# Kernel optimization log

Hardware: AMD Instinct MI355X
Metric: run time of the kernel (lower is better)

## Reference

```python
import jax, jax.numpy as jnp
import numpy as np

S_LOCAL = 3
N_HEADS = 8
EPS = 1e-6


def setup_inputs() -> dict:
    key = jax.random.key(0)
    ks = jax.random.split(key, 9)
    B, D, T, H, W = 2, 512, 96, 16, 16
    std = 0.02
    return {
        "x": jax.random.normal(ks[0], (B, D, T, H, W), dtype=jnp.float32),
        "ln_gamma": jnp.ones((D,), dtype=jnp.float32),
        "ln_beta": jnp.zeros((D,), dtype=jnp.float32),
        "Wq": jax.random.normal(ks[1], (D, D), dtype=jnp.float32) * std,
        "Wk": jax.random.normal(ks[2], (D, D), dtype=jnp.float32) * std,
        "Wv": jax.random.normal(ks[3], (D, D), dtype=jnp.float32) * std,
        "Wkl": jax.random.normal(ks[4], (D, D), dtype=jnp.float32) * std,
        "Wvl": jax.random.normal(ks[5], (D, D), dtype=jnp.float32) * std,
        "Wo": jax.random.normal(ks[6], (D, D), dtype=jnp.float32) * std,
        "q_bias": jax.random.normal(ks[7], (1, N_HEADS, 1, D // N_HEADS), dtype=jnp.float32) * std,
    }


def _unfold_windows(x, s):
    # x: [..., T] -> [..., T, s] sliding windows with zero padding s//2 each side
    p = s // 2
    xp = jnp.pad(x, [(0, 0)] * (x.ndim - 1) + [(p, p)])
    T = x.shape[-1]
    idx = jnp.arange(T)[:, None] + jnp.arange(s)[None, :]  # [T, s]
    return xp[..., idx]


def reference(x, ln_gamma, ln_beta, Wq, Wk, Wv, Wkl, Wvl, Wo, q_bias):
    B, D, T, H, W = x.shape
    nh, dh, s = N_HEADS, D // N_HEADS, S_LOCAL
    factor = dh ** (-0.5)
    N = B * H * W

    # [B,D,T,H,W] -> [N, T, D]
    xt = jnp.transpose(x, (0, 3, 4, 2, 1)).reshape(N, T, D)

    # LayerNorm over D
    mu = xt.mean(-1, keepdims=True)
    var = xt.var(-1, keepdims=True)
    xn = (xt - mu) / jnp.sqrt(var + EPS) * ln_gamma + ln_beta

    # projections -> [N, nh, T, dh]
    def heads(y):
        return jnp.transpose(y.reshape(N, T, nh, dh), (0, 2, 1, 3))

    q = heads(xn @ Wq.T) + q_bias
    k = heads(xn @ Wk.T)
    v = heads(xn @ Wv.T)

    # global attention scores [N, nh, T, T]
    attn_global = jnp.einsum('bhnd,bhgd->bhng', q, k) * factor

    # local k/v: [N, T, D] -> [N, D, T] -> windows [N, D, T, s]
    kl = jnp.transpose(xn @ Wkl.T, (0, 2, 1))
    vl = jnp.transpose(xn @ Wvl.T, (0, 2, 1))
    k_w = jnp.transpose(_unfold_windows(kl, s).reshape(N, nh, dh, T, s), (0, 1, 3, 2, 4))  # [N,nh,T,dh,s]
    v_w = jnp.transpose(_unfold_windows(vl, s).reshape(N, nh, dh, T, s), (0, 1, 3, 2, 4))

    # local mask: True where window element came from zero padding -> [T, s]
    mask_local = _unfold_windows(jnp.ones((T,), dtype=jnp.float32), s) == 0

    attn_local = jnp.einsum('bhnd,bhndl->bhnl', q, k_w)
    attn_local = jnp.where(mask_local, -jnp.inf, attn_local) * factor

    # joint softmax over [T global + s local]
    attn_map = jax.nn.softmax(jnp.concatenate([attn_global, attn_local], axis=-1), axis=-1)
    ag, al = attn_map[..., :T], attn_map[..., T:]

    x_global = jnp.einsum('bhng,bhgd->bhnd', ag, v)
    x_local = jnp.einsum('bhnl,bhndl->bhnd', al, v_w)

    out = (jnp.transpose(x_global + x_local, (0, 2, 1, 3)).reshape(N, T, D)) @ Wo.T
    return jnp.transpose(out.reshape(B, H, W, T, D), (0, 4, 3, 1, 2))
```

## Files before the change

kernel.cpp:

```cpp
#include <hip/hip_runtime.h>
#include <hip/hip_fp16.h>
#include <cstdint>
#include <cstddef>

typedef _Float16 f16;
typedef _Float16 half8 __attribute__((ext_vector_type(8)));
typedef _Float16 half4v __attribute__((ext_vector_type(4)));
typedef float floatx4 __attribute__((ext_vector_type(4)));

#define MTOT 49152
#define QSCALE 0.180336880111120426f

__device__ __forceinline__ void gload_lds16(const f16* g, f16* l) {
  __builtin_amdgcn_global_load_lds((const __attribute__((address_space(1))) void*)g,
                                   (__attribute__((address_space(3))) void*)l, 16, 0, 0);
}

__device__ __forceinline__ half8 load_h8u(const f16* p) {
  half8 v;
  __builtin_memcpy(&v, p, 16);
  return v;
}

__global__ __launch_bounds__(256) void wconv_kernel(
    const float* __restrict__ Wq, const float* __restrict__ Wk,
    const float* __restrict__ Wv, const float* __restrict__ Wkl,
    const float* __restrict__ Wvl, const float* __restrict__ Wo,
    f16* __restrict__ WQKV, f16* __restrict__ WO) {
  int idx = blockIdx.x * 256 + threadIdx.x;
  if (idx < 2560 * 512) {
    int row = idx >> 9;
    int col = idx & 511;
    int seg = row >> 9;
    int r = row & 511;
    const float* src;
    switch (seg) {
      case 0: src = Wq; break;
      case 1: src = Wk; break;
      case 2: src = Wkl; break;
      case 3: src = Wvl; break;
      default: src = Wv; break;
    }
    WQKV[idx] = (f16)src[r * 512 + col];
  }
  if (idx < 512 * 512) WO[idx] = (f16)Wo[idx];
}

__global__ __launch_bounds__(256) void ln_kernel(
    const float* __restrict__ x, const float* __restrict__ gamma,
    const float* __restrict__ beta, f16* __restrict__ XN) {
  const int hwg = blockIdx.x & 3;
  const int t   = (blockIdx.x >> 2) % 96;
  const int b   = blockIdx.x / (4 * 96);
  const int lhw = threadIdx.x & 63;
  const int dg  = threadIdx.x >> 6;
  const int hw  = hwg * 64 + lhw;
  const float* xp = x + (size_t)b * 512 * 24576 + (size_t)t * 256 + hw +
                    (size_t)dg * 128 * 24576;

  float v[128];
  float s = 0.f, s2 = 0.f;
#pragma unroll
  for (int j = 0; j < 128; ++j) {
    float u = xp[(size_t)j * 24576];
    v[j] = u;
    s += u;
    s2 += u * u;
  }
  __shared__ float S1[4][64], S2[4][64];
  S1[dg][lhw] = s;
  S2[dg][lhw] = s2;
  __syncthreads();
  s  = S1[0][lhw] + S1[1][lhw] + S1[2][lhw] + S1[3][lhw];
  s2 = S2[0][lhw] + S2[1][lhw] + S2[2][lhw] + S2[3][lhw];
  const float mean = s * (1.f / 512.f);
  float var = s2 * (1.f / 512.f) - mean * mean;
  var = fmaxf(var, 0.f);
  const float rstd = rsqrtf(var + 1e-6f);
  const int n = b * 256 + hw;
  f16* outp = XN + ((size_t)n * 96 + t) * 512 + dg * 128;
#pragma unroll
  for (int d0 = 0; d0 < 128; d0 += 8) {
    half8 buf;
#pragma unroll
    for (int j = 0; j < 8; ++j) {
      const int d = dg * 128 + d0 + j;
      buf[j] = (f16)((v[d0 + j] - mean) * rstd * gamma[d] + beta[d]);
    }
    *(half8*)(outp + d0) = buf;
  }
}

__global__ __launch_bounds__(512, 2) void gemmA_kernel(
    const f16* __restrict__ A, const f16* __restrict__ B,
    f16* __restrict__ Cqkv, const float* __restrict__ qbias) {
  __shared__ f16 LA[2][256 * 64];
  __shared__ f16 LB[2][256 * 64];
  __shared__ __align__(16) f16 esc[8][16][72];

  const int lin = blockIdx.x;
  const int cpx = (int)gridDim.x >> 3;
  const int swz = (lin & 7) * cpx + (lin >> 3);
  const int o = ((gridDim.x & 7) == 0) ? swz : lin;
  const int mt = o / 10;
  const int nt = o % 10;
  const int m0 = mt * 256;
  const int n0 = nt * 256;

  const int tid = threadIdx.x;
  const int wid = tid >> 6;
  const int lane = tid & 63;
  const int wm = wid >> 2;
  const int wn = wid & 3;
  const int l15 = lane & 15, l4 = lane >> 4;

  const int srow = tid >> 3;
  const int scol = ((tid & 7) ^ (srow & 7)) * 8;
  const f16* Abase = A + (size_t)(m0 + srow) * 512 + scol;
  const f16* Bbase = B + (size_t)(n0 + srow) * 512 + scol;

  const int cks0 = ((l4) ^ (l15 & 7)) * 8;
  const int cks1 = ((4 + l4) ^ (l15 & 7)) * 8;
  const int arow = wm * 128 + l15;
  const int brow = wn * 64 + l15;

  floatx4 acc[8][4] = {};
  half8 a_f[4][2];
  half8 b_f[4][2];

  auto stageH = [&](int slot, int kt, int mat, int h) {
    const f16* g = (mat ? Bbase : Abase) + kt * 64 + (size_t)(h * 128) * 512;
    f16* l = (mat ? LB[slot] : LA[slot]) + h * 8192 + tid * 8;
    gload_lds16(g, l);
    gload_lds16(g + (size_t)64 * 512, l + 4096);
  };

  stageH(0, 0, 0, 0); stageH(0, 0, 0, 1);
  stageH(0, 0, 1, 0); stageH(0, 0, 1, 1);
  stageH(1, 1, 0, 0);
  asm volatile("s_waitcnt vmcnt(2)" ::: "memory");
  __builtin_amdgcn_s_barrier();

#pragma unroll
  for (int kt = 0; kt < 8; ++kt) {
    const f16* As = LA[kt & 1];
    const f16* Bs = LB[kt & 1];
    const int nsl = (kt + 1) & 1;

#pragma unroll
    for (int mf2 = 0; mf2 < 4; ++mf2) {
      a_f[mf2][0] = *(const half8*)(As + (arow + mf2 * 16) * 64 + cks0);
      a_f[mf2][1] = *(const half8*)(As + (arow + mf2 * 16) * 64 + cks1);
    }
#pragma unroll
    for (int nf = 0; nf < 2; ++nf) {
      b_f[nf][0] = *(const half8*)(Bs + (brow + nf * 16) * 64 + cks0);
      b_f[nf][1] = *(const half8*)(Bs + (brow + nf * 16) * 64 + cks1);
    }
    if (kt + 1 < 8) stageH(nsl, kt + 1, 0, 1);
    __builtin_amdgcn_s_barrier();
    __builtin_amdgcn_s_setprio(1);
#pragma unroll
    for (int mf2 = 0; mf2 < 4; ++mf2)
#pragma unroll
      for (int nf2 = 0; nf2 < 2; ++nf2)
#pragma unroll
        for (int ks = 0; ks < 2; ++ks)
          acc[mf2][nf2] = __builtin_amdgcn_mfma_f32_16x16x32_f16(
              a_f[mf2][ks], b_f[nf2][ks], acc[mf2][nf2], 0, 0, 0);
    __builtin_amdgcn_s_setprio(0);
    __builtin_amdgcn_s_barrier();

#pragma unroll
    for (int nf = 2; nf < 4; ++nf) {
      b_f[nf][0] = *(const half8*)(Bs + (brow + nf * 16) * 64 + cks0);
      b_f[nf][1] = *(const half8*)(Bs + (brow + nf * 16) * 64 + cks1);
    }
    if (kt + 1 < 8) stageH(nsl, kt + 1, 1, 0);
    __builtin_amdgcn_s_barrier();
    __builtin_amdgcn_s_setprio(1);
#pragma unroll
    for (int mf2 = 0; mf2 < 4; ++mf2)
#pragma unroll
      for (int nf2 = 0; nf2 < 2; ++nf2)
#pragma unroll
        for (int ks = 0; ks < 2; ++ks)
          acc[mf2][2 + nf2] = __builtin_amdgcn_mfma_f32_16x16x32_f16(
              a_f[mf2][ks], b_f[2 + nf2][ks], acc[mf2][2 + nf2], 0, 0, 0);
    __builtin_amdgcn_s_setprio(0);
    __builtin_amdgcn_s_barrier();

#pragma unroll
    for (int mf2 = 0; mf2 < 4; ++mf2) {
      a_f[mf2][0] = *(const half8*)(As + (arow + 64 + mf2 * 16) * 64 + cks0);
      a_f[mf2][1] = *(const half8*)(As + (arow + 64 + mf2 * 16) * 64 + cks1);
    }
    if (kt + 1 < 8) stageH(nsl, kt + 1, 1, 1);
    __builtin_amdgcn_s_barrier();
    __builtin_amdgcn_s_setprio(1);
#pragma unroll
    for (int mf2 = 0; mf2 < 4; ++mf2)
#pragma unroll
      for (int nf2 = 0; nf2 < 2; ++nf2)
#pragma unroll
        for (int ks = 0; ks < 2; ++ks)
          acc[4 + mf2][nf2] = __builtin_amdgcn_mfma_f32_16x16x32_f16(
              a_f[mf2][ks], b_f[nf2][ks], acc[4 + mf2][nf2], 0, 0, 0);
    __builtin_amdgcn_s_setprio(0);
    __builtin_amdgcn_s_barrier();

    if (kt + 2 < 8) stageH(kt & 1, kt + 2, 0, 0);
    __builtin_amdgcn_s_barrier();
    __builtin_amdgcn_s_setprio(1);
#pragma unroll
    for (int mf2 = 0; mf2 < 4; ++mf2)
#pragma unroll
      for (int nf2 = 0; nf2 < 2; ++nf2)
#pragma unroll
        for (int ks = 0; ks < 2; ++ks)
          acc[4 + mf2][2 + nf2] = __builtin_amdgcn_mfma_f32_16x16x32_f16(
              a_f[mf2][ks], b_f[2 + nf2][ks], acc[4 + mf2][2 + nf2], 0, 0, 0);
    __builtin_amdgcn_s_setprio(0);
    if (kt < 6) {
      asm volatile("s_waitcnt vmcnt(2)" ::: "memory");
    } else if (kt == 6) {
      asm volatile("s_waitcnt vmcnt(0)" ::: "memory");
    }
    __builtin_amdgcn_s_barrier();
  }

  float bias[4], scl[4];
#pragma unroll
  for (int nf = 0; nf < 4; ++nf) {
    const int n = n0 + wn * 64 + nf * 16 + l15;
    const bool isq = (n < 512);
    bias[nf] = isq ? qbias[n] : 0.0f;
    scl[nf]  = isq ? QSCALE : 1.0f;
  }
  const int rrow = lane >> 2;
  const int rcg  = lane & 3;
#pragma unroll
  for (int mf = 0; mf < 8; ++mf) {
#pragma unroll
    for (int nf = 0; nf < 4; ++nf)
#pragma unroll
      for (int j = 0; j < 4; ++j)
        esc[wid][l4 * 4 + j][nf * 16 + l15] = (f16)((acc[mf][nf][j] + bias[nf]) * scl[nf]);
    asm volatile("s_waitcnt lgkmcnt(0)" ::: "memory");
    half8 v0 = *(const half8*)(&esc[wid][rrow][rcg * 16]);
    half8 v1 = *(const half8*)(&esc[wid][rrow][rcg * 16 + 8]);
    asm volatile("" ::: "memory");
    f16* dst = Cqkv + (size_t)(m0 + wm * 128 + mf * 16 + rrow) * 2560 + n0 + wn * 64 + rcg * 16;
    *(half8*)dst = v0;
    *(half8*)(dst + 8) = v1;
  }
}

__global__ __launch_bounds__(256) void gemmO_kernel(
    const f16* __restrict__ A, const f16* __restrict__ B,
    float* __restrict__ Out) {
  __shared__ f16 As[2][128 * 32];
  __shared__ f16 Bs[2][128 * 32];

  const int lin = blockIdx.x;
  const int cpx = (int)gridDim.x >> 3;
  const int o = (lin & 7) * cpx + (lin >> 3);
  const int nt = o >> 2;
  const int mt = o & 3;
  const int m0 = mt * 128;
  const int n0 = nt * 128;
  const int tid = threadIdx.x;
  const int lane = tid & 63;
  const int wid = tid >> 6;
  const int wm = wid >> 1, wn = wid & 1;
  const int l15 = lane & 15, l4 = lane >> 4;

  floatx4 acc[4][4] = {};

  const int srow = tid >> 2;
  const int skp = (((tid & 3) ^ ((tid >> 3) & 3))) * 8;
  const f16* ap = A + (size_t)(m0 + srow) * 512 + skp;
  const f16* bp = B + (size_t)(n0 + srow) * 512 + skp;

  auto stage = [&](int buf, int k0) {
    f16* asl = As[buf] + tid * 8;
    f16* bsl = Bs[buf] + tid * 8;
    gload_lds16(ap + k0, asl);
    gload_lds16(ap + (size_t)64 * 512 + k0, asl + 2048);
    gload_lds16(bp + k0, bsl);
    gload_lds16(bp + (size_t)64 * 512 + k0, bsl + 2048);
  };

  const int rc = (l4 ^ ((l15 >> 1) & 3)) * 8;

  stage(0, 0);
  __syncthreads();
  int cur = 0;
  for (int k0 = 0; k0 < 512; k0 += 32) {
    if (k0 + 32 < 512) stage(cur ^ 1, k0 + 32);
    half8 af[4], bf[4];
#pragma unroll
    for (int mf = 0; mf < 4; ++mf)
      af[mf] = *(const half8*)(As[cur] + (wm * 64 + mf * 16 + l15) * 32 + rc);
#pragma unroll
    for (int nf = 0; nf < 4; ++nf)
      bf[nf] = *(const half8*)(Bs[cur] + (wn * 64 + nf * 16 + l15) * 32 + rc);
#pragma unroll
    for (int mf = 0; mf < 4; ++mf)
#pragma unroll
      for (int nf = 0; nf < 4; ++nf)
        acc[mf][nf] = __builtin_amdgcn_mfma_f32_16x16x32_f16(af[mf], bf[nf], acc[mf][nf], 0, 0, 0);
    __syncthreads();
    cur ^= 1;
  }

  const int mbase = m0 + wm * 64;
  const int nbase = n0 + wn * 64;
#pragma unroll
  for (int nf = 0; nf < 4; ++nf) {
    const int m2 = nbase + nf * 16 + l15;
    const int bb = m2 / 24576;
    const int rem = m2 - bb * 24576;
    const int t = rem >> 8;
    const int hw = rem & 255;
    float* op = Out + ((size_t)bb * 512 * 96 + t) * 256 + hw;
#pragma unroll
    for (int mf = 0; mf < 4; ++mf) {
#pragma unroll
      for (int j = 0; j < 4; ++j) {
        const int d = mbase + mf * 16 + l4 * 4 + j;
        __builtin_nontemporal_store(acc[mf][nf][j], op + (size_t)d * 24576);
      }
    }
  }
}

__global__ __launch_bounds__(192) void attn_kernel(
    const f16* __restrict__ QKV, f16* __restrict__ AO, int n0chunk) {
  const int nn = blockIdx.x >> 3;
  const int h = blockIdx.x & 7;
  const int tid = threadIdx.x;
  const int wid = tid >> 6;
  const int lane = tid & 63;
  const int l15 = lane & 15, l4 = lane >> 4;
  const int nglob = n0chunk + nn;
  const int bb = nglob >> 8, hw = nglob & 255;

  __shared__ __align__(16) f16 VTl[64][112];
  __shared__ __align__(16) f16 VLTl[64][112];
  __shared__ __align__(16) float locS[3][16][4];
  __shared__ __align__(16) f16 pS[3][16][104];
  __shared__ __align__(16) f16 pS2[3][16][40];
  __shared__ __align__(16) f16 oesc[3][16][72];

  const f16* base = QKV + (size_t)nn * 96 * 2560;

#pragma unroll
  for (int it = 0; it < 4; ++it) {
    const int r = (tid >> 3) + it * 24;
    const int c0 = (tid & 7) * 8;
    half8 v  = *(const half8*)(base + (size_t)r * 2560 + 2048 + h * 64 + c0);
    half8 vl = *(const half8*)(base + (size_t)r * 2560 + 1536 + h * 64 + c0);
#pragma unroll
    for (int j = 0; j < 8; ++j) {
      VTl[c0 + j][r]  = v[j];
      VLTl[c0 + j][r] = vl[j];
    }
  }
  if (tid < 128) {
    half8 z = {};
    *(half8*)(&VLTl[tid >> 1][96 + (tid & 1) * 8]) = z;
  }

  half8 kb[6][2];
#pragma unroll
  for (int nf = 0; nf < 6; ++nf)
#pragma unroll
    for (int kg = 0; kg < 2; ++kg)
      kb[nf][kg] = *(const half8*)(base + (size_t)(nf * 16 + l15) * 2560 + 512 + h * 64 + kg * 32 + l4 * 8);

  __syncthreads();

  for (int mb = wid * 2; mb < wid * 2 + 2; ++mb) {
    const int t0 = mb * 16;
    const int tb = (t0 >= 2) ? (t0 - 2) : 0;
    const int d0 = t0 - 1 - tb;

    half8 aq[2], kl1[2], kl2[2];
    {
      int r1 = t0 - 1 + l15; if (r1 < 0) r1 = 0;
      int r2 = t0 + 1 + l15; if (r2 > 95) r2 = 95;
#pragma unroll
      for (int kg = 0; kg < 2; ++kg) {
        aq[kg]  = *(const half8*)(base + (size_t)(t0 + l15) * 2560 + h * 64 + kg * 32 + l4 * 8);
        kl1[kg] = *(const half8*)(base + (size_t)r1 * 2560 + 1024 + h * 64 + kg * 32 + l4 * 8);
        kl2[kg] = *(const half8*)(base + (size_t)r2 * 2560 + 1024 + h * 64 + kg * 32 + l4 * 8);
      }
    }

    floatx4 s[6] = {};
    floatx4 sl1 = {}, sl2 = {};
#pragma unroll
    for (int nf = 0; nf < 6; ++nf)
#pragma unroll
      for (int kg = 0; kg < 2; ++kg)
        s[nf] = __builtin_amdgcn_mfma_f32_16x16x32_f16(aq[kg], kb[nf][kg], s[nf], 0, 0, 0);
#pragma unroll
    for (int kg = 0; kg < 2; ++kg) {
      sl1 = __builtin_amdgcn_mfma_f32_16x16x32_f16(aq[kg], kl1[kg], sl1, 0, 0, 0);
      sl2 = __builtin_amdgcn_mfma_f32_16x16x32_f16(aq[kg], kl2[kg], sl2, 0, 0, 0);
    }

    half8 vb[4][3], vlb[4];
#pragma unroll
    for (int nf = 0; nf < 4; ++nf) {
#pragma unroll
      for (int kg = 0; kg < 3; ++kg)
        vb[nf][kg] = *(const half8*)(&VTl[nf * 16 + l15][kg * 32 + l4 * 8]);
      vlb[nf] = load_h8u(&VLTl[nf * 16 + l15][tb + l4 * 8]);
    }

    {
      half8 z = {};
      f16* pz = &pS2[wid][0][0];
      *(half8*)(pz + lane * 8) = z;
      if (lane < 16) *(half8*)(pz + 512 + lane * 8) = z;
    }
#pragma unroll
    for (int j = 0; j < 4; ++j) {
      const int r = l4 * 4 + j;
      const int s1i = l15 - r;
      if (s1i >= 0 && s1i < 3) locS[wid][r][s1i] = sl1[j];
      const int s2i = l15 + 2 - r;
      if (l15 >= 14 && s2i >= 0 && s2i < 3) locS[wid][r][s2i] = sl2[j];
    }
    __syncthreads();

#pragma unroll
    for (int j = 0; j < 4; ++j) {
      const int row = l4 * 4 + j;
      float sv[6];
#pragma unroll
      for (int nf = 0; nf < 6; ++nf) sv[nf] = s[nf][j];
      float mx = sv[0];
#pragma unroll
      for (int nf = 1; nf < 6; ++nf) mx = fmaxf(mx, sv[nf]);
      for (int off = 1; off < 16; off <<= 1) mx = fmaxf(mx, __shfl_xor(mx, off, 64));
      const float l0 = (t0 + row >= 1)  ? locS[wid][row][0] : -__builtin_inff();
      const float l1 = locS[wid][row][1];
      const float l2 = (t0 + row <= 94) ? locS[wid][row][2] : -__builtin_inff();
      mx = fmaxf(mx, fmaxf(l0, fmaxf(l1, l2)));
      float e[6], sum = 0.f;
#pragma unroll
      for (int nf = 0; nf < 6; ++nf) {
        e[nf] = exp2f(sv[nf] - mx);
        sum += e[nf];
      }
      for (int off = 1; off < 16; off <<= 1) sum += __shfl_xor(sum, off, 64);
      const float e0 = exp2f(l0 - mx), e1 = exp2f(l1 - mx), e2 = exp2f(l2 - mx);
      sum += e0 + e1 + e2;
      const float rd = 1.0f / sum;
#pragma unroll
      for (int nf = 0; nf < 6; ++nf) pS[wid][row][nf * 16 + l15] = (f16)(e[nf] * rd);
      if (l15 < 3) {
        const int w = row + l15 + d0;
        const float ev = (l15 == 0) ? e0 : ((l15 == 1) ? e1 : e2);
        if (w >= 0) pS2[wid][row][w] = (f16)(ev * rd);
      }
    }
    __syncthreads();

    floatx4 o[4] = {};
    half8 pfr[3];
#pragma unroll
    for (int kg = 0; kg < 3; ++kg)
      pfr[kg] = *(const half8*)(&pS[wid][l15][kg * 32 + l4 * 8]);
    half8 pf2 = *(const half8*)(&pS2[wid][l15][l4 * 8]);
#pragma unroll
    for (int nf = 0; nf < 4; ++nf) {
#pragma unroll
      for (int kg = 0; kg < 3; ++kg)
        o[nf] = __builtin_amdgcn_mfma_f32_16x16x32_f16(pfr[kg], vb[nf][kg], o[nf], 0, 0, 0);
      o[nf] = __builtin_amdgcn_mfma_f32_16x16x32_f16(pf2, vlb[nf], o[nf], 0, 0, 0);
    }

#pragma unroll
    for (int nf = 0; nf < 4; ++nf)
#pragma unroll
      for (int j = 0; j < 4; ++j)
        oesc[wid][l4 * 4 + j][nf * 16 + l15] = (f16)o[nf][j];
    asm volatile("s_waitcnt lgkmcnt(0)" ::: "memory");
    {
      const int rrow = lane >> 2;
      const int rcg  = lane & 3;
      half8 v0 = *(const half8*)(&oesc[wid][rrow][rcg * 16]);
      half8 v1 = *(const half8*)(&oesc[wid][rrow][rcg * 16 + 8]);
      asm volatile("" ::: "memory");
      f16* dst = AO + ((size_t)(bb * 96 + t0 + rrow) * 256 + hw) * 512 + h * 64 + rcg * 16;
      *(half8*)dst = v0;
      *(half8*)(dst + 8) = v1;
    }
  }
}

extern "C" void kernel_launch(void* const* d_in, const int* in_sizes, int n_in,
                              void* d_out, int out_size, void* d_ws, size_t ws_size,
                              hipStream_t stream) {
  (void)in_sizes; (void)n_in; (void)out_size;
  const float* x     = (const float*)d_in[0];
  const float* gamma = (const float*)d_in[1];
  const float* beta  = (const float*)d_in[2];
  const float* Wq    = (const float*)d_in[3];
  const float* Wk    = (const float*)d_in[4];
  const float* Wv    = (const float*)d_in[5];
  const float* Wkl   = (const float*)d_in[6];
  const float* Wvl   = (const float*)d_in[7];
  const float* Wo    = (const float*)d_in[8];
  const float* qb    = (const float*)d_in[9];
  float* out = (float*)d_out;

  char* ws = (char*)d_ws;
  size_t off = 0;
  auto alloc = [&](size_t bytes) -> void* {
    void* p = ws + off;
    off += (bytes + 255) & ~(size_t)255;
    return p;
  };
  f16* XN   = (f16*)alloc((size_t)MTOT * 512 * 2);
  f16* AO   = (f16*)alloc((size_t)MTOT * 512 * 2);
  f16* WQKV = (f16*)alloc((size_t)2560 * 512 * 2);
  f16* WOh  = (f16*)alloc((size_t)512 * 512 * 2);
  int cn = 512;
  while (cn > 32 && off + (size_t)cn * 96 * 2560 * 2 + 256 > ws_size)
    cn >>= 1;
  f16* QKVc = (f16*)alloc((size_t)cn * 96 * 2560 * 2);

  wconv_kernel<<<5120, 256, 0, stream>>>(Wq, Wk, Wv, Wkl, Wvl, Wo, WQKV, WOh);
  ln_kernel<<<768, 256, 0, stream>>>(x, gamma, beta, XN);

  const int nch = 512 / cn;
  for (int c = 0; c < nch; ++c) {
    const int mtiles = (cn * 96) / 256;
    gemmA_kernel<<<mtiles * 10, 512, 0, stream>>>(XN + (size_t)c * cn * 96 * 512,
                                                  WQKV, QKVc, qb);
    attn_kernel<<<cn * 8, 192, 0, stream>>>(QKVc, AO, c * cn);
  }
  gemmO_kernel<<<1536, 256, 0, stream>>>(WOh, AO, out);
}
```

Before: 391.5 us.

## Load GEMM B fragments directly from global into registers, dropping B LDS staging

The QKV projection GEMM no longer stages the weight (B) tile through shared memory. Each wave instead loads its B fragments from global memory straight into double-buffered registers one k-step ahead. This halves LDS use, which frees room for the epilogue scratch to reuse the A buffer. It also cuts the per-k-step barrier count from about eight to two. The trade-off is more VGPRs and redundant global B reads across waves sharing columns (wm=0/1), relying on L1/L2 hits, and the vmcnt bookkeeping becomes more fragile.

```diff
diff --git a/kernel.cpp b/kernel.cpp
--- a/kernel.cpp
+++ b/kernel.cpp
@@ -95,8 +95,6 @@
     const f16* __restrict__ A, const f16* __restrict__ B,
     f16* __restrict__ Cqkv, const float* __restrict__ qbias) {
   __shared__ f16 LA[2][256 * 64];
-  __shared__ f16 LB[2][256 * 64];
-  __shared__ __align__(16) f16 esc[8][16][72];
 
   const int lin = blockIdx.x;
   const int cpx = (int)gridDim.x >> 3;
@@ -117,118 +115,90 @@
   const int srow = tid >> 3;
   const int scol = ((tid & 7) ^ (srow & 7)) * 8;
   const f16* Abase = A + (size_t)(m0 + srow) * 512 + scol;
-  const f16* Bbase = B + (size_t)(n0 + srow) * 512 + scol;
 
   const int cks0 = ((l4) ^ (l15 & 7)) * 8;
   const int cks1 = ((4 + l4) ^ (l15 & 7)) * 8;
   const int arow = wm * 128 + l15;
-  const int brow = wn * 64 + l15;
+
+  const f16* bgp = B + (size_t)(n0 + wn * 64 + l15) * 512 + l4 * 8;
 
   floatx4 acc[8][4] = {};
   half8 a_f[4][2];
-  half8 b_f[4][2];
-
-  auto stageH = [&](int slot, int kt, int mat, int h) {
-    const f16* g = (mat ? Bbase : Abase) + kt * 64 + (size_t)(h * 128) * 512;
-    f16* l = (mat ? LB[slot] : LA[slot]) + h * 8192 + tid * 8;
+  half8 b_f[2][4][2];
+
+  auto stageH = [&](int slot, int kt, int h) {
+    const f16* g = Abase + kt * 64 + (size_t)(h * 128) * 512;
+    f16* l = LA[slot] + h * 8192 + tid * 8;
     gload_lds16(g, l);
     gload_lds16(g + (size_t)64 * 512, l + 4096);
   };
 
-  stageH(0, 0, 0, 0); stageH(0, 0, 0, 1);
-  stageH(0, 0, 1, 0); stageH(0, 0, 1, 1);
-  stageH(1, 1, 0, 0);
-  asm volatile("s_waitcnt vmcnt(2)" ::: "memory");
+  stageH(0, 0, 0); stageH(0, 0, 1); stageH(1, 1, 0);
+#pragma unroll
+  for (int nf = 0; nf < 4; ++nf)
+#pragma unroll
+    for (int ks = 0; ks < 2; ++ks)
+      b_f[0][nf][ks] = *(const half8*)(bgp + (size_t)(nf * 16) * 512 + ks * 32);
+  asm volatile("s_waitcnt vmcnt(10)" ::: "memory");
   __builtin_amdgcn_s_barrier();
 
 #pragma unroll
   for (int kt = 0; kt < 8; ++kt) {
     const f16* As = LA[kt & 1];
-    const f16* Bs = LB[kt & 1];
-    const int nsl = (kt + 1) & 1;
+    const int cb = kt & 1;
+    const int nb = (kt + 1) & 1;
 
 #pragma unroll
     for (int mf2 = 0; mf2 < 4; ++mf2) {
       a_f[mf2][0] = *(const half8*)(As + (arow + mf2 * 16) * 64 + cks0);
       a_f[mf2][1] = *(const half8*)(As + (arow + mf2 * 16) * 64 + cks1);
     }
-#pragma unroll
-    for (int nf = 0; nf < 2; ++nf) {
-      b_f[nf][0] = *(const half8*)(Bs + (brow + nf * 16) * 64 + cks0);
-      b_f[nf][1] = *(const half8*)(Bs + (brow + nf * 16) * 64 + cks1);
-    }
-    if (kt + 1 < 8) stageH(nsl, kt + 1, 0, 1);
-    __builtin_amdgcn_s_barrier();
+    if (kt + 1 < 8) stageH(nb, kt + 1, 1);
     __builtin_amdgcn_s_setprio(1);
 #pragma unroll
     for (int mf2 = 0; mf2 < 4; ++mf2)
 #pragma unroll
-      for (int nf2 = 0; nf2 < 2; ++nf2)
+      for (int nf = 0; nf < 4; ++nf)
 #pragma unroll
         for (int ks = 0; ks < 2; ++ks)
-          acc[mf2][nf2] = __builtin_amdgcn_mfma_f32_16x16x32_f16(
-              a_f[mf2][ks], b_f[nf2][ks], acc[mf2][nf2], 0, 0, 0);
+          acc[mf2][nf] = __builtin_amdgcn_mfma_f32_16x16x32_f16(
+              a_f[mf2][ks], b_f[cb][nf][ks], acc[mf2][nf], 0, 0, 0);
     __builtin_amdgcn_s_setprio(0);
-    __builtin_amdgcn_s_barrier();
-
-#pragma unroll
-    for (int nf = 2; nf < 4; ++nf) {
-      b_f[nf][0] = *(const half8*)(Bs + (brow + nf * 16) * 64 + cks0);
-      b_f[nf][1] = *(const half8*)(Bs + (brow + nf * 16) * 64 + cks1);
-    }
-    if (kt + 1 < 8) stageH(nsl, kt + 1, 1, 0);
-    __builtin_amdgcn_s_barrier();
-    __builtin_amdgcn_s_setprio(1);
-#pragma unroll
-    for (int mf2 = 0; mf2 < 4; ++mf2)
-#pragma unroll
-      for (int nf2 = 0; nf2 < 2; ++nf2)
-#pragma unroll
-        for (int ks = 0; ks < 2; ++ks)
-          acc[mf2][2 + nf2] = __builtin_amdgcn_mfma_f32_16x16x32_f16(
-              a_f[mf2][ks], b_f[2 + nf2][ks], acc[mf2][2 + nf2], 0, 0, 0);
-    __builtin_amdgcn_s_setprio(0);
-    __builtin_amdgcn_s_barrier();
 
 #pragma unroll
     for (int mf2 = 0; mf2 < 4; ++mf2) {
       a_f[mf2][0] = *(const half8*)(As + (arow + 64 + mf2 * 16) * 64 + cks0);
       a_f[mf2][1] = *(const half8*)(As + (arow + 64 + mf2 * 16) * 64 + cks1);
     }
-    if (kt + 1 < 8) stageH(nsl, kt + 1, 1, 1);
-    __builtin_amdgcn_s_barrier();
+    if (kt + 1 < 8) {
+#pragma unroll
+      for (int nf = 0; nf < 4; ++nf)
+#pragma unroll
+        for (int ks = 0; ks < 2; ++ks)
+          b_f[nb][nf][ks] = *(const half8*)(bgp + (size_t)(nf * 16) * 512 +
+                                            (kt + 1) * 64 + ks * 32);
+    }
     __builtin_amdgcn_s_setprio(1);
 #pragma unroll
     for (int mf2 = 0; mf2 < 4; ++mf2)
 #pragma unroll
-      for (int nf2 = 0; nf2 < 2; ++nf2)
+      for (int nf = 0; nf < 4; ++nf)
 #pragma unroll
         for (int ks = 0; ks < 2; ++ks)
-          acc[4 + mf2][nf2] = __builtin_amdgcn_mfma_f32_16x16x32_f16(
-              a_f[mf2][ks], b_f[nf2][ks], acc[4 + mf2][nf2], 0, 0, 0);
+          acc[4 + mf2][nf] = __builtin_amdgcn_mfma_f32_16x16x32_f16(
+              a_f[mf2][ks], b_f[cb][nf][ks], acc[4 + mf2][nf], 0, 0, 0);
     __builtin_amdgcn_s_setprio(0);
     __builtin_amdgcn_s_barrier();
-
-    if (kt + 2 < 8) stageH(kt & 1, kt + 2, 0, 0);
-    __builtin_amdgcn_s_barrier();
-    __builtin_amdgcn_s_setprio(1);
-#pragma unroll
-    for (int mf2 = 0; mf2 < 4; ++mf2)
-#pragma unroll
-      for (int nf2 = 0; nf2 < 2; ++nf2)
-#pragma unroll
-        for (int ks = 0; ks < 2; ++ks)
-          acc[4 + mf2][2 + nf2] = __builtin_amdgcn_mfma_f32_16x16x32_f16(
-              a_f[mf2][ks], b_f[2 + nf2][ks], acc[4 + mf2][2 + nf2], 0, 0, 0);
-    __builtin_amdgcn_s_setprio(0);
+    if (kt + 2 < 8) stageH(kt & 1, kt + 2, 0);
     if (kt < 6) {
-      asm volatile("s_waitcnt vmcnt(2)" ::: "memory");
+      asm volatile("s_waitcnt vmcnt(10)" ::: "memory");
     } else if (kt == 6) {
-      asm volatile("s_waitcnt vmcnt(0)" ::: "memory");
-    }
-    __builtin_amdgcn_s_barrier();
-  }
-
+      asm volatile("s_waitcnt vmcnt(8)" ::: "memory");
+    }
+    if (kt < 7) __builtin_amdgcn_s_barrier();
+  }
+
+  f16* escp = &LA[0][0];
   float bias[4], scl[4];
 #pragma unroll
   for (int nf = 0; nf < 4; ++nf) {
@@ -245,10 +215,11 @@
     for (int nf = 0; nf < 4; ++nf)
 #pragma unroll
       for (int j = 0; j < 4; ++j)
-        esc[wid][l4 * 4 + j][nf * 16 + l15] = (f16)((acc[mf][nf][j] + bias[nf]) * scl[nf]);
+        escp[(wid * 16 + l4 * 4 + j) * 72 + nf * 16 + l15] =
+            (f16)((acc[mf][nf][j] + bias[nf]) * scl[nf]);
     asm volatile("s_waitcnt lgkmcnt(0)" ::: "memory");
-    half8 v0 = *(const half8*)(&esc[wid][rrow][rcg * 16]);
-    half8 v1 = *(const half8*)(&esc[wid][rrow][rcg * 16 + 8]);
+    half8 v0 = *(const half8*)(&escp[(wid * 16 + rrow) * 72 + rcg * 16]);
+    half8 v1 = *(const half8*)(&escp[(wid * 16 + rrow) * 72 + rcg * 16 + 8]);
     asm volatile("" ::: "memory");
     f16* dst = Cqkv + (size_t)(m0 + wm * 128 + mf * 16 + rrow) * 2560 + n0 + wn * 64 + rcg * 16;
     *(half8*)dst = v0;
```

New measurement: 421.8 us. 1.08x slower.
